# Kernel tuning notes

Hardware: AMD Instinct MI355X
Metric: run time of the kernel (lower is better)

Reference implementation:

```python
import jax, jax.numpy as jnp
import numpy as np

N = 200000  # num nodes == num edges (edge_weight serves as both node feature and edge weight)
D_HID = 128
D_OUT = 2


def setup_inputs() -> dict:
    key = jax.random.key(0)
    ks = jax.random.split(key, 5)
    edge_index = jax.random.randint(ks[0], (2, N), 0, N, dtype=jnp.int64)
    edge_weight = jax.random.uniform(ks[1], (N,), dtype=jnp.float32)
    # Glorot-ish init for GCNConv linear layers (bias=True by default in PyG)
    W1 = jax.random.normal(ks[2], (1, D_HID), dtype=jnp.float32) * (1.0 / np.sqrt(1))
    W2 = jax.random.normal(ks[3], (D_HID, D_HID), dtype=jnp.float32) * (1.0 / np.sqrt(D_HID))
    W3 = jax.random.normal(ks[4], (D_HID, D_OUT), dtype=jnp.float32) * (1.0 / np.sqrt(D_HID))
    b1 = jnp.zeros((D_HID,), dtype=jnp.float32)
    b2 = jnp.zeros((D_HID,), dtype=jnp.float32)
    b3 = jnp.zeros((D_OUT,), dtype=jnp.float32)
    return {"edge_index": edge_index, "edge_weight": edge_weight,
            "W1": W1, "b1": b1, "W2": W2, "b2": b2, "W3": W3, "b3": b3}


def reference(edge_index, edge_weight, W1, b1, W2, b2, W3, b3):
    n = edge_weight.shape[0]
    src, dst = edge_index[0], edge_index[1]
    # GCN symmetric normalization with self-loops (PyG gcn_norm, fill_value=1.0)
    loops = jnp.arange(n)
    src_f = jnp.concatenate([src, loops])            # [2N]
    dst_f = jnp.concatenate([dst, loops])            # [2N]
    w_f = jnp.concatenate([edge_weight, jnp.ones((n,), edge_weight.dtype)])
    deg = jax.ops.segment_sum(w_f, dst_f, num_segments=n)
    dinv = jnp.where(deg > 0, deg ** -0.5, 0.0)
    norm = dinv[src_f] * w_f * dinv[dst_f]           # [2N], identical for all layers

    def conv(x, W, b):
        h = x @ W                                    # linear transform first (out <= in path)
        msg = h[src_f] * norm[:, None]               # gather + edge scale
        return jax.ops.segment_sum(msg, dst_f, num_segments=n) + b  # scatter-add aggregate

    x = edge_weight[:, None]                         # node features = edge weights, [N,1]
    x = jax.nn.relu(conv(x, W1, b1))
    x = jax.nn.relu(conv(x, W2, b2))
    x = jax.nn.relu(conv(x, W3, b3))
    return jax.nn.log_softmax(x, axis=1)
```

## Files before the change

### kernel.cpp

```cpp
#include <hip/hip_runtime.h>

#define NN 200000
#define NE 200000
#define DH 128
#define CAP 16
#define NTILES (NN / 64)
#define L2BLK ((NTILES + 1) / 2)

typedef float f32x4 __attribute__((ext_vector_type(4)));
typedef _Float16 f16x8 __attribute__((ext_vector_type(8)));
#define AS1 __attribute__((address_space(1)))
#define AS3 __attribute__((address_space(3)))

__device__ __forceinline__ unsigned pack2h(float a, float b) {
  unsigned short ua = __builtin_bit_cast(unsigned short, (_Float16)a);
  unsigned short ub = __builtin_bit_cast(unsigned short, (_Float16)b);
  return (unsigned)ua | ((unsigned)ub << 16);
}
__device__ __forceinline__ float deg_of(int p) {
  return (float)(((unsigned)p) & 0x03FFFFFFu) * (1.0f / 1048576.0f) + 1.0f;
}
__device__ __forceinline__ int cnt_of(int p) { return (int)(((unsigned)p) >> 26); }

__global__ void k_build(const int* __restrict__ src, const int* __restrict__ dst,
                        const float* __restrict__ ew, int* __restrict__ pdeg,
                        int2* __restrict__ slot,
                        const float* __restrict__ W2, unsigned* __restrict__ w2g) {
  int tid = threadIdx.x;
  int e = blockIdx.x * 256 + tid;
  if (e < NE) {
    int d = dst[e];
    int sv = src[e];
    float w = ew[e];
    int addend = __float2int_rn(w * 1048576.0f) | (1 << 26);
    int old = atomicAdd(&pdeg[d], addend);
    int r = (int)(((unsigned)old) >> 26);
    if (r < CAP) slot[d * CAP + r] = make_int2(sv, __float_as_int(w));
  }
  if (blockIdx.x < 32) {
    int gid = blockIdx.x * 256 + tid;
    int fkc = gid >> 8, l = (gid >> 2) & 63, dd = gid & 3;
    int n = (fkc >> 2) * 16 + (l & 15);
    int dwp = (fkc & 3) * 16 + (l >> 4) * 4 + dd;
    w2g[gid] = pack2h(W2[(2 * dwp) * DH + n], W2[(2 * dwp + 1) * DH + n]);
  }
}

__global__ void k_nodes(const float* __restrict__ ew, const int* __restrict__ pdeg,
                        int2* __restrict__ slot, float* __restrict__ s) {
  int d = blockIdx.x * 256 + threadIdx.x;
  if (d >= NN) return;
  int p = pdeg[d];
  float dv = rsqrtf(deg_of(p));
  int cnt = min(cnt_of(p), CAP);
  const int4* sp = (const int4*)(slot + d * CAP);
  int4 a = sp[0], b = sp[1];
  int2 sl[4] = {{a.x, a.y}, {a.z, a.w}, {b.x, b.y}, {b.z, b.w}};
  int n4 = min(cnt, 4);
  int sidx[4];
  bool v[4];
#pragma unroll
  for (int u = 0; u < 4; u++) { v[u] = u < n4; sidx[u] = v[u] ? sl[u].x : d; }
  float dg[4], we[4];
#pragma unroll
  for (int u = 0; u < 4; u++) { dg[u] = deg_of(pdeg[sidx[u]]); we[u] = ew[sidx[u]]; }
  float acc = 0.f;
#pragma unroll
  for (int u = 0; u < 4; u++) {
    if (v[u]) {
      float wdvs = __int_as_float(sl[u].y) * rsqrtf(dg[u]);
      acc = fmaf(wdvs, we[u], acc);
      slot[d * CAP + u] = make_int2(sl[u].x, __float_as_int(wdvs * dv));
    }
  }
  for (int j = 4; j < cnt; ++j) {
    int2 t = slot[d * CAP + j];
    float wdvs = __int_as_float(t.y) * rsqrtf(deg_of(pdeg[t.x]));
    acc = fmaf(wdvs, ew[t.x], acc);
    slot[d * CAP + j] = make_int2(t.x, __float_as_int(wdvs * dv));
  }
  s[d] = dv * fmaf(dv, ew[d], acc);
}

__global__ __launch_bounds__(256, 3) void k_layer2(
    const float* __restrict__ s, const int* __restrict__ pdeg,
    const int2* __restrict__ slot,
    const float* __restrict__ W1, const float* __restrict__ b1,
    const float* __restrict__ b2, const float* __restrict__ W3,
    const unsigned* __restrict__ w2g, float* __restrict__ h3) {
  __shared__ __align__(16) char smem[49152];
  unsigned* w2t = (unsigned*)smem;
  uint4* tAf = (uint4*)(smem + 32768);
  float* eS = (float*)(smem + 32768);
  float* eN = (float*)(smem + 32768 + 3328);
  int tid = threadIdx.x;
  int wv = tid >> 6;

#pragma unroll
  for (int i = 0; i < 8; ++i)
    __builtin_amdgcn_global_load_lds(
        (const AS1 unsigned*)(w2g + i * 1024 + tid * 4),
        (AS3 unsigned*)(w2t + i * 1024 + wv * 256), 16, 0, 0);

  int lr15 = tid & 15, q = (tid >> 4) & 3;
  int l = tid & 63, g = l >> 4, lr = l & 15;
  int myn = wv * 16 + lr15;
  float w1r[32], b1r[32];
#pragma unroll
  for (int c = 0; c < 32; c++) { w1r[c] = W1[q * 32 + c]; b1r[c] = b1[q * 32 + c]; }

  for (int t = 0; t < 2; ++t) {
    int tile = blockIdx.x + t * L2BLK;
    if (tile >= NTILES) break;
    int base = tile * 64;
    int d = base + myn;

    int2 sl3[3];
#pragma unroll
    for (int it = 0; it < 3; ++it) {
      int idx = it * 256 + tid;
      int nl = idx / 12, j = idx - nl * 12;
      sl3[it] = slot[base * CAP + nl * CAP + j];
    }
    int pd = pdeg[d];
    float sd = s[d];
    float dvd = rsqrtf(deg_of(pd));
    float sn = dvd * dvd;
    int mycnt = min(cnt_of(pd), CAP);

    if (t > 0) __syncthreads();
#pragma unroll
    for (int it = 0; it < 3; ++it) {
      int idx = it * 256 + tid;
      int nl = idx / 12, j = idx - nl * 12;
      if ((unsigned)sl3[it].x < NN) {
        eS[nl * 13 + j] = s[sl3[it].x];
        eN[nl * 13 + j] = __int_as_float(sl3[it].y);
      }
    }

    float acc[32];
#pragma unroll
    for (int c = 0; c < 32; c++)
      acc[c] = sn * fmaxf(fmaf(sd, w1r[c], b1r[c]), 0.f);
    __syncthreads();

    int c12 = min(mycnt, 12);
    for (int j = 0; j < c12; ++j) {
      float ss = eS[myn * 13 + j], nr = eN[myn * 13 + j];
#pragma unroll
      for (int c = 0; c < 32; c++)
        acc[c] = fmaf(nr, fmaxf(fmaf(ss, w1r[c], b1r[c]), 0.f), acc[c]);
    }
    if (mycnt > 12) {
      for (int j = 12; j < mycnt; ++j) {
        int2 sl = slot[d * CAP + j];
        float ss = s[sl.x];
        float nr = __int_as_float(sl.y);
#pragma unroll
        for (int c = 0; c < 32; c++)
          acc[c] = fmaf(nr, fmaxf(fmaf(ss, w1r[c], b1r[c]), 0.f), acc[c]);
      }
    }
    __syncthreads();

#pragma unroll
    for (int hi = 0; hi < 4; ++hi) {
      uint4 u;
      u.x = pack2h(acc[8 * hi + 0], acc[8 * hi + 1]);
      u.y = pack2h(acc[8 * hi + 2], acc[8 * hi + 3]);
      u.z = pack2h(acc[8 * hi + 4], acc[8 * hi + 5]);
      u.w = pack2h(acc[8 * hi + 6], acc[8 * hi + 7]);
      tAf[(wv * 4 + q) * 64 + hi * 16 + lr15] = u;
    }
    __syncthreads();

    f32x4 acc8[8];
#pragma unroll
    for (int f = 0; f < 8; f++) acc8[f] = (f32x4){0.f, 0.f, 0.f, 0.f};
#pragma unroll
    for (int kc = 0; kc < 4; kc++) {
      f16x8 av = __builtin_bit_cast(f16x8, tAf[(wv * 4 + kc) * 64 + l]);
#pragma unroll
      for (int f = 0; f < 8; f++) {
        f16x8 bv = __builtin_bit_cast(f16x8, *(const uint4*)(w2t + ((f * 4 + kc) * 64 + l) * 4));
        acc8[f] = __builtin_amdgcn_mfma_f32_16x16x32_f16(av, bv, acc8[f], 0, 0, 0);
      }
    }

    float p0[4] = {0.f, 0.f, 0.f, 0.f}, p1[4] = {0.f, 0.f, 0.f, 0.f};
#pragma unroll
    for (int f = 0; f < 8; f++) {
      int n = f * 16 + lr;
      float bb = b2[n];
      float2 w3v = ((const float2*)W3)[n];
#pragma unroll
      for (int r = 0; r < 4; r++) {
        float v = fmaxf(acc8[f][r] + bb, 0.f);
        p0[r] = fmaf(v, w3v.x, p0[r]);
        p1[r] = fmaf(v, w3v.y, p1[r]);
      }
    }
#pragma unroll
    for (int r = 0; r < 4; r++) {
#pragma unroll
      for (int m = 8; m; m >>= 1) {
        p0[r] += __shfl_xor(p0[r], m);
        p1[r] += __shfl_xor(p1[r], m);
      }
    }
    if (lr == 0) {
#pragma unroll
      for (int r = 0; r < 4; r++) {
        int node = base + wv * 16 + g * 4 + r;
        ((float2*)h3)[node] = make_float2(p0[r], p1[r]);
      }
    }
  }
}

__global__ void k_final(const float* __restrict__ h3, const int* __restrict__ pdeg,
                        const int2* __restrict__ slot, const float* __restrict__ b3,
                        float* __restrict__ out) {
  int d = blockIdx.x * 256 + threadIdx.x;
  if (d >= NN) return;
  int p = pdeg[d];
  float dvd = rsqrtf(deg_of(p));
  float sn = dvd * dvd;
  int cnt = min(cnt_of(p), CAP);
  const int4* sp = (const int4*)(slot + d * CAP);
  int4 a = sp[0], b = sp[1];
  int2 sl[4] = {{a.x, a.y}, {a.z, a.w}, {b.x, b.y}, {b.z, b.w}};
  float2 hv = ((const float2*)h3)[d];
  float y0 = sn * hv.x, y1 = sn * hv.y;
  int n4 = min(cnt, 4);
  int idx4[4];
  bool v[4];
#pragma unroll
  for (int u = 0; u < 4; u++) { v[u] = u < n4; idx4[u] = v[u] ? sl[u].x : d; }
  float2 hs[4];
#pragma unroll
  for (int u = 0; u < 4; u++) hs[u] = ((const float2*)h3)[idx4[u]];
#pragma unroll
  for (int u = 0; u < 4; u++) {
    if (v[u]) {
      float nr = __int_as_float(sl[u].y);
      y0 = fmaf(nr, hs[u].x, y0);
      y1 = fmaf(nr, hs[u].y, y1);
    }
  }
  for (int j = 4; j < cnt; ++j) {
    int2 t = slot[d * CAP + j];
    float nr = __int_as_float(t.y);
    float2 h = ((const float2*)h3)[t.x];
    y0 = fmaf(nr, h.x, y0);
    y1 = fmaf(nr, h.y, y1);
  }
  float z0 = fmaxf(y0 + b3[0], 0.f);
  float z1 = fmaxf(y1 + b3[1], 0.f);
  float m = fmaxf(z0, z1);
  float lse = m + logf(expf(z0 - m) + expf(z1 - m));
  out[2 * d] = z0 - lse;
  out[2 * d + 1] = z1 - lse;
}

extern "C" void kernel_launch(void* const* d_in, const int* in_sizes, int n_in,
                              void* d_out, int out_size, void* d_ws, size_t ws_size,
                              hipStream_t stream) {
  const int* ei = (const int*)d_in[0];
  const int* srcp = ei;
  const int* dstp = ei + NE;
  const float* ew = (const float*)d_in[1];
  const float* W1 = (const float*)d_in[2];
  const float* b1 = (const float*)d_in[3];
  const float* W2 = (const float*)d_in[4];
  const float* b2 = (const float*)d_in[5];
  const float* W3 = (const float*)d_in[6];
  const float* b3 = (const float*)d_in[7];
  float* out = (float*)d_out;

  char* ws = (char*)d_ws;
  size_t off = 0;
  auto alloc = [&](size_t bytes) -> void* {
    void* p = ws + off;
    off = (off + bytes + 255) & ~size_t(255);
    return p;
  };
  int* pdeg = (int*)alloc(NN * 4);
  size_t zero_bytes = off;
  int2* slot = (int2*)alloc((size_t)NN * CAP * 8);
  float* s = (float*)alloc(NN * 4);
  unsigned* w2g = (unsigned*)alloc(8192 * 4);
  float* h3 = (float*)alloc(NN * 2 * 4);
  (void)ws_size; (void)in_sizes; (void)n_in; (void)out_size;

  const int nbE = (NE + 255) / 256;
  const int nbN = (NN + 255) / 256;

  hipMemsetAsync(pdeg, 0, zero_bytes, stream);
  k_build<<<nbE, 256, 0, stream>>>(srcp, dstp, ew, pdeg, slot, W2, w2g);
  k_nodes<<<nbN, 256, 0, stream>>>(ew, pdeg, slot, s);
  k_layer2<<<L2BLK, 256, 0, stream>>>(s, pdeg, slot, W1, b1, b2, W3, w2g, h3);
  k_final<<<nbN, 256, 0, stream>>>(h3, pdeg, slot, b3, out);
}
```

Baseline: 131.7 us.

## Widen unrolled neighbor gathers to 8 and prefetch both tiles' slots in layer2

k_nodes and k_final now issue eight independent neighbor gathers up front instead of four, which gives more memory-level parallelism for nodes with higher in-degree. In k_layer2 the staged per-node neighbor list in shared memory shrinks from 12 to 8 entries (stride 9). The slot entries and neighbor s values for both tiles a block handles are loaded before the main loop, so the second tile's gathers overlap the first tile's compute. Nodes with more than 8 neighbors take the slower uncached global-memory path, and the extra prefetched values raise register pressure.

```diff
diff --git a/kernel.cpp b/kernel.cpp
--- a/kernel.cpp
+++ b/kernel.cpp
@@ -54,26 +54,27 @@
   float dv = rsqrtf(deg_of(p));
   int cnt = min(cnt_of(p), CAP);
   const int4* sp = (const int4*)(slot + d * CAP);
-  int4 a = sp[0], b = sp[1];
-  int2 sl[4] = {{a.x, a.y}, {a.z, a.w}, {b.x, b.y}, {b.z, b.w}};
-  int n4 = min(cnt, 4);
-  int sidx[4];
-  bool v[4];
-#pragma unroll
-  for (int u = 0; u < 4; u++) { v[u] = u < n4; sidx[u] = v[u] ? sl[u].x : d; }
-  float dg[4], we[4];
-#pragma unroll
-  for (int u = 0; u < 4; u++) { dg[u] = deg_of(pdeg[sidx[u]]); we[u] = ew[sidx[u]]; }
+  int4 q0 = sp[0], q1 = sp[1], q2 = sp[2], q3 = sp[3];
+  int2 sl[8] = {{q0.x, q0.y}, {q0.z, q0.w}, {q1.x, q1.y}, {q1.z, q1.w},
+                {q2.x, q2.y}, {q2.z, q2.w}, {q3.x, q3.y}, {q3.z, q3.w}};
+  int n8 = min(cnt, 8);
+  int sidx[8];
+  bool v[8];
+#pragma unroll
+  for (int u = 0; u < 8; u++) { v[u] = u < n8; sidx[u] = v[u] ? sl[u].x : d; }
+  float dg[8], we[8];
+#pragma unroll
+  for (int u = 0; u < 8; u++) { dg[u] = deg_of(pdeg[sidx[u]]); we[u] = ew[sidx[u]]; }
   float acc = 0.f;
 #pragma unroll
-  for (int u = 0; u < 4; u++) {
+  for (int u = 0; u < 8; u++) {
     if (v[u]) {
       float wdvs = __int_as_float(sl[u].y) * rsqrtf(dg[u]);
       acc = fmaf(wdvs, we[u], acc);
       slot[d * CAP + u] = make_int2(sl[u].x, __float_as_int(wdvs * dv));
     }
   }
-  for (int j = 4; j < cnt; ++j) {
+  for (int j = 8; j < cnt; ++j) {
     int2 t = slot[d * CAP + j];
     float wdvs = __int_as_float(t.y) * rsqrtf(deg_of(pdeg[t.x]));
     acc = fmaf(wdvs, ew[t.x], acc);
@@ -92,7 +93,7 @@
   unsigned* w2t = (unsigned*)smem;
   uint4* tAf = (uint4*)(smem + 32768);
   float* eS = (float*)(smem + 32768);
-  float* eN = (float*)(smem + 32768 + 3328);
+  float* eN = (float*)(smem + 32768 + 2304);
   int tid = threadIdx.x;
   int wv = tid >> 6;
 
@@ -105,58 +106,79 @@
   int lr15 = tid & 15, q = (tid >> 4) & 3;
   int l = tid & 63, g = l >> 4, lr = l & 15;
   int myn = wv * 16 + lr15;
+  int snl = tid >> 3, sj = tid & 7;
+
+  int tile0 = blockIdx.x, tile1 = blockIdx.x + L2BLK;
+  bool has1 = tile1 < NTILES;
+  int t1c = has1 ? tile1 : tile0;
+
+  int2 sl[2][2];
+  bool vld[2][2];
+#pragma unroll
+  for (int tt = 0; tt < 2; ++tt) {
+    int tb = (tt ? t1c : tile0) * 64;
+#pragma unroll
+    for (int it = 0; it < 2; ++it) {
+      int nl = it * 32 + snl;
+      int2 sv = slot[tb * CAP + nl * CAP + sj];
+      sl[tt][it] = sv;
+      vld[tt][it] = (unsigned)sv.x < NN;
+    }
+  }
+  int d0 = tile0 * 64 + myn, d1 = t1c * 64 + myn;
+  int pd0 = pdeg[d0], pd1 = pdeg[d1];
+  float sd0 = s[d0], sd1 = s[d1];
+  float sG[2][2];
+#pragma unroll
+  for (int tt = 0; tt < 2; ++tt)
+#pragma unroll
+    for (int it = 0; it < 2; ++it)
+      sG[tt][it] = s[vld[tt][it] ? sl[tt][it].x : 0];
+
   float w1r[32], b1r[32];
 #pragma unroll
   for (int c = 0; c < 32; c++) { w1r[c] = W1[q * 32 + c]; b1r[c] = b1[q * 32 + c]; }
 
   for (int t = 0; t < 2; ++t) {
-    int tile = blockIdx.x + t * L2BLK;
-    if (tile >= NTILES) break;
+    if (t && !has1) break;
+    int tile = t ? tile1 : tile0;
     int base = tile * 64;
-    int d = base + myn;
-
-    int2 sl3[3];
-#pragma unroll
-    for (int it = 0; it < 3; ++it) {
-      int idx = it * 256 + tid;
-      int nl = idx / 12, j = idx - nl * 12;
-      sl3[it] = slot[base * CAP + nl * CAP + j];
-    }
-    int pd = pdeg[d];
-    float sd = s[d];
+    int pd = t ? pd1 : pd0;
+    float sd = t ? sd1 : sd0;
+
+    if (t) __syncthreads();
+#pragma unroll
+    for (int it = 0; it < 2; ++it) {
+      int nl = it * 32 + snl;
+      if (vld[t][it]) {
+        eS[nl * 9 + sj] = sG[t][it];
+        eN[nl * 9 + sj] = __int_as_float(sl[t][it].y);
+      }
+    }
+
     float dvd = rsqrtf(deg_of(pd));
     float sn = dvd * dvd;
     int mycnt = min(cnt_of(pd), CAP);
 
-    if (t > 0) __syncthreads();
-#pragma unroll
-    for (int it = 0; it < 3; ++it) {
-      int idx = it * 256 + tid;
-      int nl = idx / 12, j = idx - nl * 12;
-      if ((unsigned)sl3[it].x < NN) {
-        eS[nl * 13 + j] = s[sl3[it].x];
-        eN[nl * 13 + j] = __int_as_float(sl3[it].y);
-      }
-    }
-
     float acc[32];
 #pragma unroll
     for (int c = 0; c < 32; c++)
       acc[c] = sn * fmaxf(fmaf(sd, w1r[c], b1r[c]), 0.f);
     __syncthreads();
 
-    int c12 = min(mycnt, 12);
-    for (int j = 0; j < c12; ++j) {
-      float ss = eS[myn * 13 + j], nr = eN[myn * 13 + j];
+    int c8 = min(mycnt, 8);
+    for (int j = 0; j < c8; ++j) {
+      float ss = eS[myn * 9 + j], nr = eN[myn * 9 + j];
 #pragma unroll
       for (int c = 0; c < 32; c++)
         acc[c] = fmaf(nr, fmaxf(fmaf(ss, w1r[c], b1r[c]), 0.f), acc[c]);
     }
-    if (mycnt > 12) {
-      for (int j = 12; j < mycnt; ++j) {
-        int2 sl = slot[d * CAP + j];
-        float ss = s[sl.x];
-        float nr = __int_as_float(sl.y);
+    if (mycnt > 8) {
+      int dd = base + myn;
+      for (int j = 8; j < mycnt; ++j) {
+        int2 sv = slot[dd * CAP + j];
+        float ss = s[sv.x];
+        float nr = __int_as_float(sv.y);
 #pragma unroll
         for (int c = 0; c < 32; c++)
           acc[c] = fmaf(nr, fmaxf(fmaf(ss, w1r[c], b1r[c]), 0.f), acc[c]);
@@ -229,27 +251,28 @@
   float sn = dvd * dvd;
   int cnt = min(cnt_of(p), CAP);
   const int4* sp = (const int4*)(slot + d * CAP);
-  int4 a = sp[0], b = sp[1];
-  int2 sl[4] = {{a.x, a.y}, {a.z, a.w}, {b.x, b.y}, {b.z, b.w}};
+  int4 q0 = sp[0], q1 = sp[1], q2 = sp[2], q3 = sp[3];
+  int2 sl[8] = {{q0.x, q0.y}, {q0.z, q0.w}, {q1.x, q1.y}, {q1.z, q1.w},
+                {q2.x, q2.y}, {q2.z, q2.w}, {q3.x, q3.y}, {q3.z, q3.w}};
   float2 hv = ((const float2*)h3)[d];
   float y0 = sn * hv.x, y1 = sn * hv.y;
-  int n4 = min(cnt, 4);
-  int idx4[4];
-  bool v[4];
-#pragma unroll
-  for (int u = 0; u < 4; u++) { v[u] = u < n4; idx4[u] = v[u] ? sl[u].x : d; }
-  float2 hs[4];
-#pragma unroll
-  for (int u = 0; u < 4; u++) hs[u] = ((const float2*)h3)[idx4[u]];
-#pragma unroll
-  for (int u = 0; u < 4; u++) {
+  int n8 = min(cnt, 8);
+  int idx8[8];
+  bool v[8];
+#pragma unroll
+  for (int u = 0; u < 8; u++) { v[u] = u < n8; idx8[u] = v[u] ? sl[u].x : d; }
+  float2 hs[8];
+#pragma unroll
+  for (int u = 0; u < 8; u++) hs[u] = ((const float2*)h3)[idx8[u]];
+#pragma unroll
+  for (int u = 0; u < 8; u++) {
     if (v[u]) {
       float nr = __int_as_float(sl[u].y);
       y0 = fmaf(nr, hs[u].x, y0);
       y1 = fmaf(nr, hs[u].y, y1);
     }
   }
-  for (int j = 4; j < cnt; ++j) {
+  for (int j = 8; j < cnt; ++j) {
     int2 t = slot[d * CAP + j];
     float nr = __int_as_float(t.y);
     float2 h = ((const float2*)h3)[t.x];
```

New measurement: 173.8 us. +32.0%, slower.
